# Kernel tuning notes

Hardware: AMD Instinct MI355X
Metric: run time of the kernel (lower is better)

Reference implementation:

```python
import jax, jax.numpy as jnp
import numpy as np

SIZES = [11793, 2948, 737, 184]   # vertices per mesh level, fine -> coarse
SPIRAL = [20, 14, 12, 9]          # spiral length per level
FILT = [128, 128, 64, 3]          # filters_dec[0]
LATENT = 128
BATCH = 16


def setup_inputs() -> dict:
    key = jax.random.key(0)
    ks = jax.random.split(key, 12)
    V = [s + 1 for s in SIZES]  # +1 dummy vertex per level
    inp = {}
    inp["z"] = jax.random.normal(ks[0], (BATCH, LATENT), jnp.float32)
    # dense upsampling matrices: level k+1 -> level k
    inp["U0"] = jax.random.normal(ks[1], (V[0], V[1]), jnp.float32) * 0.02
    inp["U1"] = jax.random.normal(ks[2], (V[1], V[2]), jnp.float32) * 0.02
    inp["U2"] = jax.random.normal(ks[3], (V[2], V[3]), jnp.float32) * 0.02
    # spiral index tables per level (shared across batch, values in [0, V))
    inp["S0"] = jax.random.randint(ks[4], (V[0], SPIRAL[0]), 0, V[0], dtype=jnp.int32)
    inp["S1"] = jax.random.randint(ks[5], (V[1], SPIRAL[1]), 0, V[1], dtype=jnp.int32)
    inp["S2"] = jax.random.randint(ks[6], (V[2], SPIRAL[2]), 0, V[2], dtype=jnp.int32)
    # fc_latent_dec: latent -> (sizes[-1]+1)*filters_dec[0][0]
    inp["Wfc"] = jax.random.normal(ks[7], (LATENT, V[3] * FILT[0]), jnp.float32) * 0.02
    inp["bfc"] = jnp.zeros((V[3] * FILT[0],), jnp.float32)
    # SpiralConv linear weights, stored (K*F_in, F_out), K-major flatten as in torch
    inp["W0"] = jax.random.normal(ks[8], (SPIRAL[2] * FILT[0], FILT[1]), jnp.float32) * 0.02
    inp["b0"] = jnp.zeros((FILT[1],), jnp.float32)
    inp["W1"] = jax.random.normal(ks[9], (SPIRAL[1] * FILT[1], FILT[2]), jnp.float32) * 0.02
    inp["b1"] = jnp.zeros((FILT[2],), jnp.float32)
    inp["W2"] = jax.random.normal(ks[10], (SPIRAL[0] * FILT[2], FILT[3]), jnp.float32) * 0.02
    inp["b2"] = jnp.zeros((FILT[3],), jnp.float32)
    return inp


def spiral_conv(x, S, W, b, elu):
    # x: (B, V, F); S: (V, K) vertex indices into the same level
    B, V, F = x.shape
    K = S.shape[1]
    g = jnp.take(x, S.reshape(-1), axis=1).reshape(B, V, K * F)  # gather, K-major flatten
    out = g @ W + b  # (B, V, F_out)
    if elu:
        out = jax.nn.elu(out)
    # zero out the dummy (last) vertex, as in Neural3DMM's zero_padding mask
    return out.at[:, -1, :].set(0.0)


def reference(z, U0, U1, U2, S0, S1, S2, Wfc, bfc, W0, b0, W1, b1, W2, b2):
    B = z.shape[0]
    x = (z @ Wfc + bfc).reshape(B, SIZES[-1] + 1, FILT[0])  # (B, 185, 128)
    x = jnp.einsum('vw,bwf->bvf', U2, x)                    # upsample -> (B, 738, 128)
    x = spiral_conv(x, S2, W0, b0, True)                    # (B, 738, 128)
    x = jnp.einsum('vw,bwf->bvf', U1, x)                    # (B, 2949, 128)
    x = spiral_conv(x, S1, W1, b1, True)                    # (B, 2949, 64)
    x = jnp.einsum('vw,bwf->bvf', U0, x)                    # (B, 11794, 64)
    x = spiral_conv(x, S0, W2, b2, False)                   # identity act -> (B, 11794, 3)
    return x
```

## Files before the change

### kernel.cpp

```cpp
#include <hip/hip_runtime.h>
#include <cmath>


#define NB 16

typedef __attribute__((ext_vector_type(8))) short bf16x8;
typedef __attribute__((ext_vector_type(4))) float f32x4;

__device__ __forceinline__ unsigned short f2bf(float x) {
    union { float f; unsigned u; } v; v.f = x;
    unsigned r = v.u + 0x7FFFu + ((v.u >> 16) & 1u);
    return (unsigned short)(r >> 16);
}
__device__ __forceinline__ void gload16(const void* src, void* dst) {
    __builtin_amdgcn_global_load_lds(
        (const __attribute__((address_space(1))) unsigned int*)src,
        (__attribute__((address_space(3))) unsigned int*)dst, 16, 0, 0);
}

__global__ __launch_bounds__(256) void cvt_ub(const float* __restrict__ src,
                                              unsigned short* __restrict__ dst,
                                              int V, int W, int Wp) {
    int k = blockIdx.x * 256 + threadIdx.x;
    int row = blockIdx.y;
    if (k >= Wp) return;
    float v = (row < V && k < W) ? src[(size_t)row * W + k] : 0.f;
    dst[(size_t)row * Wp + k] = f2bf(v);
}
__global__ __launch_bounds__(256) void cvt_wT(const float* __restrict__ w,
                                              unsigned short* __restrict__ wT,
                                              int K, int N, int total) {
    int id = blockIdx.x * 256 + threadIdx.x;
    if (id >= total) return;
    int n = id / K, k = id - n * K;
    wT[id] = f2bf(w[(size_t)k * N + n]);
}
__global__ __launch_bounds__(256) void cvt_w2(const float* __restrict__ w,
                                              unsigned short* __restrict__ wt) {
    int id = blockIdx.x * 256 + threadIdx.x;
    if (id >= 16 * 1288) return;
    int n = id / 1288, k = id - n * 1288;
    float v = (n < 3 && k < 1280) ? w[(size_t)k * 3 + n] : 0.f;
    wt[id] = f2bf(v);
}
__global__ __launch_bounds__(256) void cvt_sT(const int* __restrict__ S,
                                              int* __restrict__ ST,
                                              int V, int K, int total) {
    int id = blockIdx.x * 256 + threadIdx.x;
    if (id >= total) return;
    int k = id / V, v = id - k * V;
    ST[id] = S[(size_t)v * K + k];
}
__global__ __launch_bounds__(256) void zero16(int4* __restrict__ p, int n16) {
    int id = blockIdx.x * 256 + threadIdx.x;
    if (id < n16) p[id] = make_int4(0, 0, 0, 0);
}

__global__ __launch_bounds__(256) void fc_kernel(const float* __restrict__ z,
                                                 const float* __restrict__ Wfc,
                                                 const float* __restrict__ bfc,
                                                 unsigned short* __restrict__ x3T) {
    const int N = 185 * 128;
    __shared__ float zs[NB * 128];
    int t = threadIdx.x;
    for (int i = t; i < NB * 128; i += 256) zs[i] = z[i];
    __syncthreads();
    int n = blockIdx.x * 256 + t;
    if (n >= N) return;
    float acc[NB];
#pragma unroll
    for (int b = 0; b < NB; ++b) acc[b] = 0.f;
    for (int k = 0; k < 128; ++k) {
        float w = Wfc[k * N + n];
#pragma unroll
        for (int b = 0; b < NB; ++b) acc[b] = fmaf(zs[b * 128 + k], w, acc[b]);
    }
    float bv = bfc[n];
    int f = n & 127, v = n >> 7;
#pragma unroll
    for (int b = 0; b < NB; ++b)
        x3T[(size_t)(b * 128 + f) * 192 + v] = f2bf(acc[b] + bv);
}

template<int FSH, int VP>
__global__ __launch_bounds__(256) void ups_mfma(
    const unsigned short* __restrict__ Ub, const unsigned short* __restrict__ xT,
    unsigned short* __restrict__ out,
    int WpA, int WpB, int nsteps, int gxsh, int q) {
    const int F = 1 << FSH;
    __shared__ __align__(16) unsigned short As[3][128 * 32];
    __shared__ __align__(16) unsigned short Bs[3][128 * 32];
    const int t = threadIdx.x;
    const int wv = t >> 6, lane = t & 63;
    const int lr = lane & 15;

    const int flat = blockIdx.x;
    const int wg = (flat & 7) * q + (flat >> 3);
    const int m0 = (wg >> gxsh) * 128;
    const int n0 = (wg & ((1 << gxsh) - 1)) * 128;

    const int srow = lane >> 2;
    const int schunk = (((lane & 3) - ((lane >> 3) & 3)) & 3) * 8;
    const int ii0 = wv * 2, ii1 = wv * 2 + 1;
    const unsigned short* asrc0 = Ub + (size_t)(m0 + ii0 * 16 + srow) * WpA + schunk;
    const unsigned short* asrc1 = Ub + (size_t)(m0 + ii1 * 16 + srow) * WpA + schunk;
    const unsigned short* bsrc0 = xT + (size_t)(n0 + ii0 * 16 + srow) * WpB + schunk;
    const unsigned short* bsrc1 = xT + (size_t)(n0 + ii1 * 16 + srow) * WpB + schunk;

    const int fslot = (((lane >> 4) + (lr >> 1)) & 3) * 8;
    const int wrow = (wv >> 1) * 64;
    const int wcol = (wv & 1) * 64;
    const int u0 = wv * 1024;

    f32x4 acc[4][4];
#pragma unroll
    for (int i = 0; i < 4; ++i)
#pragma unroll
        for (int j = 0; j < 4; ++j) acc[i][j] = {0.f, 0.f, 0.f, 0.f};

#define UPS_STAGE(off_, B_)                                             \
    {                                                                   \
        gload16(asrc0 + (off_), &As[B_][u0]);                           \
        gload16(bsrc0 + (off_), &Bs[B_][u0]);                           \
        gload16(asrc1 + (off_), &As[B_][u0 + 512]);                     \
        gload16(bsrc1 + (off_), &Bs[B_][u0 + 512]);                     \
    }
#define UPS_COMPUTE(B_)                                                 \
    {                                                                   \
        bf16x8 af[4], bg[4];                                            \
        _Pragma("unroll")                                               \
        for (int mt = 0; mt < 4; ++mt)                                  \
            af[mt] = *(const bf16x8*)&As[B_][(wrow + mt * 16 + lr) * 32 + fslot]; \
        _Pragma("unroll")                                               \
        for (int nt = 0; nt < 4; ++nt)                                  \
            bg[nt] = *(const bf16x8*)&Bs[B_][(wcol + nt * 16 + lr) * 32 + fslot]; \
        _Pragma("unroll")                                               \
        for (int mt = 0; mt < 4; ++mt)                                  \
            _Pragma("unroll")                                           \
            for (int nt = 0; nt < 4; ++nt)                              \
                acc[mt][nt] = __builtin_amdgcn_mfma_f32_16x16x32_bf16(  \
                    af[mt], bg[nt], acc[mt][nt], 0, 0, 0);              \
    }
#define UPS_WAIT4 asm volatile("s_waitcnt vmcnt(4)" ::: "memory"); __builtin_amdgcn_s_barrier();
#define UPS_WAIT0 asm volatile("s_waitcnt vmcnt(0)" ::: "memory"); __builtin_amdgcn_s_barrier();

    UPS_STAGE(0, 0);
    UPS_STAGE(32, 1);
    UPS_WAIT4;

    const int m = nsteps / 3;
    for (int it = 0; it < m - 1; ++it) {
        UPS_STAGE(64, 2);  UPS_COMPUTE(0); UPS_WAIT4;
        UPS_STAGE(96, 0);  UPS_COMPUTE(1); UPS_WAIT4;
        UPS_STAGE(128, 1); UPS_COMPUTE(2); UPS_WAIT4;
        asrc0 += 96; asrc1 += 96; bsrc0 += 96; bsrc1 += 96;
    }
    UPS_STAGE(64, 2);
    UPS_COMPUTE(0); UPS_WAIT4;
    UPS_COMPUTE(1); UPS_WAIT0;
    UPS_COMPUTE(2);
#undef UPS_STAGE
#undef UPS_COMPUTE
#undef UPS_WAIT4
#undef UPS_WAIT0

#pragma unroll
    for (int mt = 0; mt < 4; ++mt) {
        const int vb = m0 + wrow + mt * 16 + (lane >> 4) * 4;
#pragma unroll
        for (int nt = 0; nt < 4; ++nt) {
            const int col = n0 + wcol + nt * 16 + lr;
            const int b = col >> FSH, f = col & (F - 1);
            unsigned short* op = out + (size_t)b * VP * F + f;
#pragma unroll
            for (int j = 0; j < 4; ++j)
                op[(size_t)(vb + j) * F] = f2bf(acc[mt][nt][j]);
        }
    }
}

template<int VP>
__global__ __launch_bounds__(64) void conv_mfma(
    const unsigned short* __restrict__ xu, const int* __restrict__ ST,
    const unsigned short* __restrict__ WT, const float* __restrict__ bias,
    unsigned short* __restrict__ outT,
    int VT, int Ksp, int Kdim, int nsteps, int Fout) {
    __shared__ __align__(16) unsigned short As[2][32 * 32];
    __shared__ __align__(16) unsigned short Bs[2][64 * 32];
    const int lane = threadIdx.x;
    const int lr = lane & 15;
    const int m0 = blockIdx.x * 32;
    const int n0 = blockIdx.y * 64;
    const int b = m0 / VP;
    const int v0 = m0 - b * VP;
    const unsigned short* xb = xu + (((size_t)b * VP) << 7);

    const int arow = lane >> 1;
    const int h = lane & 1;
    const int vg = (v0 + arow < VT) ? (v0 + arow) : (VT - 1);
    const int schunk = (((lane & 3) - ((lane >> 3) & 3)) & 3) * 8;
    const int fslot = (((lane >> 4) + (lr >> 1)) & 3) * 8;
    int sw0 = arow * 32 + (((2 * h + 0 + ((lane >> 2) & 3)) & 3) * 8);
    int sw1 = arow * 32 + (((2 * h + 1 + ((lane >> 2) & 3)) & 3) * 8);

    int s_c = 0;
    int idx_c = ST[vg];
    int idx_n = ST[(size_t)VT + vg];

    f32x4 acc[2][4];
#pragma unroll
    for (int i = 0; i < 2; ++i)
#pragma unroll
        for (int j = 0; j < 4; ++j) acc[i][j] = {0.f, 0.f, 0.f, 0.f};

#define CONV_COMPUTE(B_)                                                \
    {                                                                   \
        bf16x8 af[2], bg[4];                                            \
        _Pragma("unroll")                                               \
        for (int mt = 0; mt < 2; ++mt)                                  \
            af[mt] = *(const bf16x8*)&As[B_][(mt * 16 + lr) * 32 + fslot]; \
        _Pragma("unroll")                                               \
        for (int nt = 0; nt < 4; ++nt)                                  \
            bg[nt] = *(const bf16x8*)&Bs[B_][(nt * 16 + lr) * 32 + fslot]; \
        _Pragma("unroll")                                               \
        for (int mt = 0; mt < 2; ++mt)                                  \
            _Pragma("unroll")                                           \
            for (int nt = 0; nt < 4; ++nt)                              \
                acc[mt][nt] = __builtin_amdgcn_mfma_f32_16x16x32_bf16(  \
                    af[mt], bg[nt], acc[mt][nt], 0, 0, 0);              \
    }
#define CONV_BODY(tn_, CUR_, NXT_)                                      \
    {                                                                   \
        const int k0 = (tn_) * 32;                                      \
        const int sn = k0 >> 7;                                         \
        const int idx = (sn != s_c) ? idx_n : idx_c;                    \
        const unsigned short* p = xb + (((size_t)idx) << 7) + (k0 & 127) + h * 16; \
        bf16x8 g0 = *(const bf16x8*)(p);                                \
        bf16x8 g1 = *(const bf16x8*)(p + 8);                            \
        _Pragma("unroll")                                               \
        for (int i = 0; i < 4; ++i) {                                   \
            const int n = n0 + i * 16 + (lane >> 2);                    \
            gload16(WT + (size_t)n * Kdim + k0 + schunk, &Bs[NXT_][i * 512]); \
        }                                                               \
        if (sn != s_c) {                                                \
            idx_c = idx_n; s_c = sn;                                    \
            if (s_c + 1 < Ksp) idx_n = ST[(size_t)(s_c + 1) * VT + vg]; \
        }                                                               \
        CONV_COMPUTE(CUR_);                                             \
        *(bf16x8*)&As[NXT_][sw0] = g0;                                  \
        *(bf16x8*)&As[NXT_][sw1] = g1;                                  \
        __syncthreads();                                                \
    }

    {
        const unsigned short* p = xb + (((size_t)idx_c) << 7) + h * 16;
        bf16x8 g0 = *(const bf16x8*)(p);
        bf16x8 g1 = *(const bf16x8*)(p + 8);
#pragma unroll
        for (int i = 0; i < 4; ++i) {
            const int n = n0 + i * 16 + (lane >> 2);
            gload16(WT + (size_t)n * Kdim + schunk, &Bs[0][i * 512]);
        }
        *(bf16x8*)&As[0][sw0] = g0;
        *(bf16x8*)&As[0][sw1] = g1;
    }
    __syncthreads();

    for (int ts = 0; ts + 2 < nsteps; ts += 2) {
        CONV_BODY(ts + 1, 0, 1);
        CONV_BODY(ts + 2, 1, 0);
    }
    CONV_BODY(nsteps - 1, 0, 1);
    CONV_COMPUTE(1);
#undef CONV_BODY
#undef CONV_COMPUTE

#pragma unroll
    for (int nt = 0; nt < 4; ++nt) {
        const int n = n0 + nt * 16 + lr;
        const float bv = bias[n];
        unsigned short* op = outT + (size_t)(b * Fout + n) * VP;
#pragma unroll
        for (int mt = 0; mt < 2; ++mt) {
            const int v = v0 + mt * 16 + (lane >> 4) * 4;
            ushort4 stv;
#pragma unroll
            for (int j = 0; j < 4; ++j) {
                float val = acc[mt][nt][j] + bv;
                val = val > 0.f ? val : expm1f(val);
                if (v + j == VT - 1) val = 0.f;
                ((unsigned short*)&stv)[j] = f2bf(val);
            }
            *(ushort4*)(op + v) = stv;
        }
    }
}

__global__ __launch_bounds__(64) void out_mfma(
    const unsigned short* __restrict__ xu, const int* __restrict__ ST,
    const unsigned short* __restrict__ W2T, const float* __restrict__ b2,
    float* __restrict__ out) {
    const int VT = 11794, VP = 11904, TPB = 372;
    __shared__ __align__(16) unsigned short As[2][32 * 32];
    const int lane = threadIdx.x;
    const int lr = lane & 15;
    const int lko = (lane >> 4) * 8;
    const int bm = blockIdx.x;
    const int b = bm / TPB;
    const int v0 = (bm - b * TPB) * 32;
    const unsigned short* xb = xu + ((size_t)b * VP << 6);

    const int arow = lane >> 1;
    const int h = lane & 1;
    const int v = v0 + arow;
    const int vg = v < VT ? v : VT - 1;
    int sw0 = arow * 32 + (((2 * h + 0 + ((lane >> 2) & 3)) & 3) * 8);
    int sw1 = arow * 32 + (((2 * h + 1 + ((lane >> 2) & 3)) & 3) * 8);
    const int fslot = (((lane >> 4) + (lr >> 1)) & 3) * 8;

    int s_c = 0;
    int idx_c = ST[vg];
    int idx_n = ST[VT + vg];

    f32x4 acc[2];
    acc[0] = {0.f, 0.f, 0.f, 0.f};
    acc[1] = {0.f, 0.f, 0.f, 0.f};

    const unsigned short* wrow = W2T + (size_t)lr * 1288 + lko;
    bf16x8 bg_c = *(const bf16x8*)(wrow);

#define OUT_COMPUTE(B_)                                                 \
    {                                                                   \
        bf16x8 af[2];                                                   \
        _Pragma("unroll")                                               \
        for (int mt = 0; mt < 2; ++mt)                                  \
            af[mt] = *(const bf16x8*)&As[B_][(mt * 16 + lr) * 32 + fslot]; \
        _Pragma("unroll")                                               \
        for (int mt = 0; mt < 2; ++mt)                                  \
            acc[mt] = __builtin_amdgcn_mfma_f32_16x16x32_bf16(af[mt], bg_c, acc[mt], 0, 0, 0); \
    }
#define OUT_BODY(tn_, CUR_, NXT_)                                       \
    {                                                                   \
        const int k0 = (tn_) * 32;                                      \
        const int sn = k0 >> 6;                                         \
        const int idx = (sn != s_c) ? idx_n : idx_c;                    \
        const unsigned short* p = xb + (((size_t)idx) << 6) + (k0 & 63) + h * 16; \
        bf16x8 g0 = *(const bf16x8*)(p);                                \
        bf16x8 g1 = *(const bf16x8*)(p + 8);                            \
        bf16x8 bg_n = *(const bf16x8*)(wrow + k0);                      \
        if (sn != s_c) {                                                \
            idx_c = idx_n; s_c = sn;                                    \
            if (s_c + 1 < 20) idx_n = ST[(size_t)(s_c + 1) * VT + vg];  \
        }                                                               \
        OUT_COMPUTE(CUR_);                                              \
        bg_c = bg_n;                                                    \
        *(bf16x8*)&As[NXT_][sw0] = g0;                                  \
        *(bf16x8*)&As[NXT_][sw1] = g1;                                  \
        __syncthreads();                                                \
    }

    {
        const unsigned short* p = xb + ((size_t)idx_c << 6) + h * 16;
        bf16x8 g0 = *(const bf16x8*)(p);
        bf16x8 g1 = *(const bf16x8*)(p + 8);
        *(bf16x8*)&As[0][sw0] = g0;
        *(bf16x8*)&As[0][sw1] = g1;
    }
    __syncthreads();

    const int nsteps = 40;
    for (int ts = 0; ts + 2 < nsteps; ts += 2) {
        OUT_BODY(ts + 1, 0, 1);
        OUT_BODY(ts + 2, 1, 0);
    }
    OUT_BODY(nsteps - 1, 0, 1);
    OUT_COMPUTE(1);
#undef OUT_BODY
#undef OUT_COMPUTE

    if (lr < 3) {
        const float bv = b2[lr];
#pragma unroll
        for (int mt = 0; mt < 2; ++mt) {
#pragma unroll
            for (int j = 0; j < 4; ++j) {
                const int vv = v0 + mt * 16 + (lane >> 4) * 4 + j;
                if (vv < VT) {
                    float val = acc[mt][j] + bv;
                    if (vv == VT - 1) val = 0.f;
                    out[((size_t)b * VT + vv) * 3 + lr] = val;
                }
            }
        }
    }
}

extern "C" void kernel_launch(void* const* d_in, const int* in_sizes, int n_in,
                              void* d_out, int out_size, void* d_ws, size_t ws_size,
                              hipStream_t stream) {
    const float* z   = (const float*)d_in[0];
    const float* U0  = (const float*)d_in[1];
    const float* U1  = (const float*)d_in[2];
    const float* U2  = (const float*)d_in[3];
    const int*   S0  = (const int*)d_in[4];
    const int*   S1  = (const int*)d_in[5];
    const int*   S2  = (const int*)d_in[6];
    const float* Wfc = (const float*)d_in[7];
    const float* bfc = (const float*)d_in[8];
    const float* W0  = (const float*)d_in[9];
    const float* b0  = (const float*)d_in[10];
    const float* W1  = (const float*)d_in[11];
    const float* b1  = (const float*)d_in[12];
    const float* W2  = (const float*)d_in[13];
    const float* b2  = (const float*)d_in[14];
    float* out = (float*)d_out;

    char* ws = (char*)d_ws;
    unsigned short* Ub0 = (unsigned short*)(ws + 0);
    unsigned short* Ub1 = (unsigned short*)(ws + 70852608);
    unsigned short* Ub2 = (unsigned short*)(ws + 75571200);
    unsigned short* x3T = (unsigned short*)(ws + 75866112);
    unsigned short* x2u = (unsigned short*)(ws + 76652544);
    unsigned short* x2T = (unsigned short*)(ws + 79798272);
    unsigned short* x1u = (unsigned short*)(ws + 82944000);
    unsigned short* x1T = (unsigned short*)(ws + 95526912);
    unsigned short* x0u = (unsigned short*)(ws + 101818368);
    unsigned short* W0T = (unsigned short*)(ws + 126197760);
    unsigned short* W1T = (unsigned short*)(ws + 126590976);
    int* S1T = (int*)(ws + 126820352);
    int* S2T = (int*)(ws + 126985504);
    int* S0T = (int*)(ws + 127020928);
    unsigned short* W2T = (unsigned short*)(ws + 127964448);

    cvt_ub<<<dim3(12, 11904), 256, 0, stream>>>(U0, Ub0, 11794, 2949, 2976);
    cvt_ub<<<dim3(3, 3072), 256, 0, stream>>>(U1, Ub1, 2949, 738, 768);
    cvt_ub<<<dim3(1, 768), 256, 0, stream>>>(U2, Ub2, 738, 185, 192);
    cvt_wT<<<dim3((128 * 1536 + 255) / 256), 256, 0, stream>>>(W0, W0T, 1536, 128, 128 * 1536);
    cvt_wT<<<dim3((64 * 1792 + 255) / 256), 256, 0, stream>>>(W1, W1T, 1792, 64, 64 * 1792);
    cvt_w2<<<dim3((16 * 1288 + 255) / 256), 256, 0, stream>>>(W2, W2T);
    cvt_sT<<<dim3((14 * 2949 + 255) / 256), 256, 0, stream>>>(S1, S1T, 2949, 14, 14 * 2949);
    cvt_sT<<<dim3((12 * 738 + 255) / 256), 256, 0, stream>>>(S2, S2T, 738, 12, 12 * 738);
    cvt_sT<<<dim3((20 * 11794 + 255) / 256), 256, 0, stream>>>(S0, S0T, 11794, 20, 20 * 11794);
    zero16<<<dim3(192), 256, 0, stream>>>((int4*)x3T, 2048 * 192 * 2 / 16);

    fc_kernel<<<dim3((185 * 128 + 255) / 256), 256, 0, stream>>>(z, Wfc, bfc, x3T);
    ups_mfma<7, 768><<<dim3(96), 256, 0, stream>>>(Ub2, x3T, x2u, 192, 192, 6, 4, 12);
    conv_mfma<768><<<dim3(384, 2), 64, 0, stream>>>(x2u, S2T, W0T, b0, x2T, 738, 12, 1536, 48, 128);
    ups_mfma<7, 3072><<<dim3(384), 256, 0, stream>>>(Ub1, x2T, x1u, 768, 768, 24, 4, 48);
    conv_mfma<3072><<<dim3(1536, 1), 64, 0, stream>>>(x1u, S1T, W1T, b1, x1T, 2949, 14, 1792, 56, 64);
    ups_mfma<6, 11904><<<dim3(744), 256, 0, stream>>>(Ub0, x1T, x0u, 2976, 3072, 93, 3, 93);
    out_mfma<<<dim3(16 * 372), 64, 0, stream>>>(x0u, S0T, W2T, b2, out);
}
```

Before: 375.4 us.

## Replace LDS-staged spiral conv kernels with direct-register gather MFMA kernels

After: 420.2 us. 11.9% more time.

```diff
diff --git a/kernel.cpp b/kernel.cpp
--- a/kernel.cpp
+++ b/kernel.cpp
@@ -179,33 +179,25 @@
     }
 }
 
-template<int VP>
-__global__ __launch_bounds__(64) void conv_mfma(
+__global__ __launch_bounds__(256) void conv_nolds(
     const unsigned short* __restrict__ xu, const int* __restrict__ ST,
     const unsigned short* __restrict__ WT, const float* __restrict__ bias,
     unsigned short* __restrict__ outT,
-    int VT, int Ksp, int Kdim, int nsteps, int Fout) {
-    __shared__ __align__(16) unsigned short As[2][32 * 32];
-    __shared__ __align__(16) unsigned short Bs[2][64 * 32];
-    const int lane = threadIdx.x;
-    const int lr = lane & 15;
-    const int m0 = blockIdx.x * 32;
+    int VT, int VP, int Ksp, int Kdim, int Fout) {
+    const int t = threadIdx.x, wv = t >> 6, lane = t & 63;
+    const int lr = lane & 15, lko = (lane >> 4) * 8;
+    const int m0 = blockIdx.x * 128 + wv * 32;
     const int n0 = blockIdx.y * 64;
     const int b = m0 / VP;
     const int v0 = m0 - b * VP;
-    const unsigned short* xb = xu + (((size_t)b * VP) << 7);
-
-    const int arow = lane >> 1;
-    const int h = lane & 1;
-    const int vg = (v0 + arow < VT) ? (v0 + arow) : (VT - 1);
-    const int schunk = (((lane & 3) - ((lane >> 3) & 3)) & 3) * 8;
-    const int fslot = (((lane >> 4) + (lr >> 1)) & 3) * 8;
-    int sw0 = arow * 32 + (((2 * h + 0 + ((lane >> 2) & 3)) & 3) * 8);
-    int sw1 = arow * 32 + (((2 * h + 1 + ((lane >> 2) & 3)) & 3) * 8);
-
-    int s_c = 0;
-    int idx_c = ST[vg];
-    int idx_n = ST[(size_t)VT + vg];
+    const unsigned short* xb = xu + ((size_t)b * VP << 7);
+    const int r0 = v0 + lr, r1 = v0 + 16 + lr;
+    const int vg0 = r0 < VT ? r0 : VT - 1;
+    const int vg1 = r1 < VT ? r1 : VT - 1;
+    const unsigned short* wb0 = WT + (size_t)(n0 + lr) * Kdim + lko;
+    const unsigned short* wb1 = wb0 + (size_t)16 * Kdim;
+    const unsigned short* wb2 = wb0 + (size_t)32 * Kdim;
+    const unsigned short* wb3 = wb0 + (size_t)48 * Kdim;
 
     f32x4 acc[2][4];
 #pragma unroll
@@ -213,67 +205,36 @@
 #pragma unroll
         for (int j = 0; j < 4; ++j) acc[i][j] = {0.f, 0.f, 0.f, 0.f};
 
-#define CONV_COMPUTE(B_)                                                \
-    {                                                                   \
-        bf16x8 af[2], bg[4];                                            \
-        _Pragma("unroll")                                               \
-        for (int mt = 0; mt < 2; ++mt)                                  \
-            af[mt] = *(const bf16x8*)&As[B_][(mt * 16 + lr) * 32 + fslot]; \
-        _Pragma("unroll")                                               \
-        for (int nt = 0; nt < 4; ++nt)                                  \
-            bg[nt] = *(const bf16x8*)&Bs[B_][(nt * 16 + lr) * 32 + fslot]; \
-        _Pragma("unroll")                                               \
-        for (int mt = 0; mt < 2; ++mt)                                  \
-            _Pragma("unroll")                                           \
-            for (int nt = 0; nt < 4; ++nt)                              \
-                acc[mt][nt] = __builtin_amdgcn_mfma_f32_16x16x32_bf16(  \
-                    af[mt], bg[nt], acc[mt][nt], 0, 0, 0);              \
-    }
-#define CONV_BODY(tn_, CUR_, NXT_)                                      \
-    {                                                                   \
-        const int k0 = (tn_) * 32;                                      \
-        const int sn = k0 >> 7;                                         \
-        const int idx = (sn != s_c) ? idx_n : idx_c;                    \
-        const unsigned short* p = xb + (((size_t)idx) << 7) + (k0 & 127) + h * 16; \
-        bf16x8 g0 = *(const bf16x8*)(p);                                \
-        bf16x8 g1 = *(const bf16x8*)(p + 8);                            \
-        _Pragma("unroll")                                               \
-        for (int i = 0; i < 4; ++i) {                                   \
-            const int n = n0 + i * 16 + (lane >> 2);                    \
-            gload16(WT + (size_t)n * Kdim + k0 + schunk, &Bs[NXT_][i * 512]); \
-        }                                                               \
-        if (sn != s_c) {                                                \
-            idx_c = idx_n; s_c = sn;                                    \
-            if (s_c + 1 < Ksp) idx_n = ST[(size_t)(s_c + 1) * VT + vg]; \
-        }                                                               \
-        CONV_COMPUTE(CUR_);                                             \
-        *(bf16x8*)&As[NXT_][sw0] = g0;                                  \
-        *(bf16x8*)&As[NXT_][sw1] = g1;                                  \
-        __syncthreads();                                                \
-    }
-
-    {
-        const unsigned short* p = xb + (((size_t)idx_c) << 7) + h * 16;
-        bf16x8 g0 = *(const bf16x8*)(p);
-        bf16x8 g1 = *(const bf16x8*)(p + 8);
-#pragma unroll
-        for (int i = 0; i < 4; ++i) {
-            const int n = n0 + i * 16 + (lane >> 2);
-            gload16(WT + (size_t)n * Kdim + schunk, &Bs[0][i * 512]);
-        }
-        *(bf16x8*)&As[0][sw0] = g0;
-        *(bf16x8*)&As[0][sw1] = g1;
-    }
-    __syncthreads();
-
-    for (int ts = 0; ts + 2 < nsteps; ts += 2) {
-        CONV_BODY(ts + 1, 0, 1);
-        CONV_BODY(ts + 2, 1, 0);
-    }
-    CONV_BODY(nsteps - 1, 0, 1);
-    CONV_COMPUTE(1);
-#undef CONV_BODY
-#undef CONV_COMPUTE
+    int idx0 = ST[vg0];
+    int idx1 = ST[vg1];
+    for (int ks = 0; ks < Ksp; ++ks) {
+        int ni0 = idx0, ni1 = idx1;
+        if (ks + 1 < Ksp) {
+            ni0 = ST[(size_t)(ks + 1) * VT + vg0];
+            ni1 = ST[(size_t)(ks + 1) * VT + vg1];
+        }
+        const unsigned short* pa0 = xb + ((size_t)idx0 << 7) + lko;
+        const unsigned short* pa1 = xb + ((size_t)idx1 << 7) + lko;
+        const int kb = ks << 7;
+#pragma unroll
+        for (int sub = 0; sub < 4; ++sub) {
+            bf16x8 a0 = *(const bf16x8*)(pa0 + sub * 32);
+            bf16x8 a1 = *(const bf16x8*)(pa1 + sub * 32);
+            bf16x8 g0 = *(const bf16x8*)(wb0 + kb + sub * 32);
+            bf16x8 g1 = *(const bf16x8*)(wb1 + kb + sub * 32);
+            bf16x8 g2 = *(const bf16x8*)(wb2 + kb + sub * 32);
+            bf16x8 g3 = *(const bf16x8*)(wb3 + kb + sub * 32);
+            acc[0][0] = __builtin_amdgcn_mfma_f32_16x16x32_bf16(a0, g0, acc[0][0], 0, 0, 0);
+            acc[1][0] = __builtin_amdgcn_mfma_f32_16x16x32_bf16(a1, g0, acc[1][0], 0, 0, 0);
+            acc[0][1] = __builtin_amdgcn_mfma_f32_16x16x32_bf16(a0, g1, acc[0][1], 0, 0, 0);
+            acc[1][1] = __builtin_amdgcn_mfma_f32_16x16x32_bf16(a1, g1, acc[1][1], 0, 0, 0);
+            acc[0][2] = __builtin_amdgcn_mfma_f32_16x16x32_bf16(a0, g2, acc[0][2], 0, 0, 0);
+            acc[1][2] = __builtin_amdgcn_mfma_f32_16x16x32_bf16(a1, g2, acc[1][2], 0, 0, 0);
+            acc[0][3] = __builtin_amdgcn_mfma_f32_16x16x32_bf16(a0, g3, acc[0][3], 0, 0, 0);
+            acc[1][3] = __builtin_amdgcn_mfma_f32_16x16x32_bf16(a1, g3, acc[1][3], 0, 0, 0);
+        }
+        idx0 = ni0; idx1 = ni1;
+    }
 
 #pragma unroll
     for (int nt = 0; nt < 4; ++nt) {
@@ -296,92 +257,57 @@
     }
 }
 
-__global__ __launch_bounds__(64) void out_mfma(
+__global__ __launch_bounds__(256) void out_nolds(
     const unsigned short* __restrict__ xu, const int* __restrict__ ST,
     const unsigned short* __restrict__ W2T, const float* __restrict__ b2,
     float* __restrict__ out) {
-    const int VT = 11794, VP = 11904, TPB = 372;
-    __shared__ __align__(16) unsigned short As[2][32 * 32];
-    const int lane = threadIdx.x;
-    const int lr = lane & 15;
-    const int lko = (lane >> 4) * 8;
-    const int bm = blockIdx.x;
-    const int b = bm / TPB;
-    const int v0 = (bm - b * TPB) * 32;
+    const int VT = 11794, VP = 11904;
+    const int t = threadIdx.x, wv = t >> 6, lane = t & 63;
+    const int lr = lane & 15, lko = (lane >> 4) * 8;
+    const int m0 = blockIdx.x * 256 + wv * 64;
+    const int b = m0 / VP;
+    const int v0 = m0 - b * VP;
     const unsigned short* xb = xu + ((size_t)b * VP << 6);
-
-    const int arow = lane >> 1;
-    const int h = lane & 1;
-    const int v = v0 + arow;
-    const int vg = v < VT ? v : VT - 1;
-    int sw0 = arow * 32 + (((2 * h + 0 + ((lane >> 2) & 3)) & 3) * 8);
-    int sw1 = arow * 32 + (((2 * h + 1 + ((lane >> 2) & 3)) & 3) * 8);
-    const int fslot = (((lane >> 4) + (lr >> 1)) & 3) * 8;
-
-    int s_c = 0;
-    int idx_c = ST[vg];
-    int idx_n = ST[VT + vg];
-
-    f32x4 acc[2];
-    acc[0] = {0.f, 0.f, 0.f, 0.f};
-    acc[1] = {0.f, 0.f, 0.f, 0.f};
-
+    int vg[4];
+#pragma unroll
+    for (int mt = 0; mt < 4; ++mt) {
+        int r = v0 + mt * 16 + lr;
+        vg[mt] = r < VT ? r : VT - 1;
+    }
     const unsigned short* wrow = W2T + (size_t)lr * 1288 + lko;
-    bf16x8 bg_c = *(const bf16x8*)(wrow);
-
-#define OUT_COMPUTE(B_)                                                 \
-    {                                                                   \
-        bf16x8 af[2];                                                   \
-        _Pragma("unroll")                                               \
-        for (int mt = 0; mt < 2; ++mt)                                  \
-            af[mt] = *(const bf16x8*)&As[B_][(mt * 16 + lr) * 32 + fslot]; \
-        _Pragma("unroll")                                               \
-        for (int mt = 0; mt < 2; ++mt)                                  \
-            acc[mt] = __builtin_amdgcn_mfma_f32_16x16x32_bf16(af[mt], bg_c, acc[mt], 0, 0, 0); \
-    }
-#define OUT_BODY(tn_, CUR_, NXT_)                                       \
-    {                                                                   \
-        const int k0 = (tn_) * 32;                                      \
-        const int sn = k0 >> 6;                                         \
-        const int idx = (sn != s_c) ? idx_n : idx_c;                    \
-        const unsigned short* p = xb + (((size_t)idx) << 6) + (k0 & 63) + h * 16; \
-        bf16x8 g0 = *(const bf16x8*)(p);                                \
-        bf16x8 g1 = *(const bf16x8*)(p + 8);                            \
-        bf16x8 bg_n = *(const bf16x8*)(wrow + k0);                      \
-        if (sn != s_c) {                                                \
-            idx_c = idx_n; s_c = sn;                                    \
-            if (s_c + 1 < 20) idx_n = ST[(size_t)(s_c + 1) * VT + vg];  \
-        }                                                               \
-        OUT_COMPUTE(CUR_);                                              \
-        bg_c = bg_n;                                                    \
-        *(bf16x8*)&As[NXT_][sw0] = g0;                                  \
-        *(bf16x8*)&As[NXT_][sw1] = g1;                                  \
-        __syncthreads();                                                \
-    }
-
-    {
-        const unsigned short* p = xb + ((size_t)idx_c << 6) + h * 16;
-        bf16x8 g0 = *(const bf16x8*)(p);
-        bf16x8 g1 = *(const bf16x8*)(p + 8);
-        *(bf16x8*)&As[0][sw0] = g0;
-        *(bf16x8*)&As[0][sw1] = g1;
-    }
-    __syncthreads();
-
-    const int nsteps = 40;
-    for (int ts = 0; ts + 2 < nsteps; ts += 2) {
-        OUT_BODY(ts + 1, 0, 1);
-        OUT_BODY(ts + 2, 1, 0);
-    }
-    OUT_BODY(nsteps - 1, 0, 1);
-    OUT_COMPUTE(1);
-#undef OUT_BODY
-#undef OUT_COMPUTE
+
+    f32x4 acc[4];
+#pragma unroll
+    for (int i = 0; i < 4; ++i) acc[i] = {0.f, 0.f, 0.f, 0.f};
+
+    int i0 = ST[vg[0]], i1 = ST[vg[1]], i2 = ST[vg[2]], i3 = ST[vg[3]];
+    for (int ks = 0; ks < 20; ++ks) {
+        int n0i = i0, n1i = i1, n2i = i2, n3i = i3;
+        if (ks + 1 < 20) {
+            const int* srow = ST + (size_t)(ks + 1) * VT;
+            n0i = srow[vg[0]]; n1i = srow[vg[1]];
+            n2i = srow[vg[2]]; n3i = srow[vg[3]];
+        }
+        const int kb = ks << 6;
+#pragma unroll
+        for (int sub = 0; sub < 2; ++sub) {
+            bf16x8 bgv = *(const bf16x8*)(wrow + kb + sub * 32);
+            bf16x8 a0 = *(const bf16x8*)(xb + ((size_t)i0 << 6) + sub * 32 + lko);
+            bf16x8 a1 = *(const bf16x8*)(xb + ((size_t)i1 << 6) + sub * 32 + lko);
+            bf16x8 a2 = *(const bf16x8*)(xb + ((size_t)i2 << 6) + sub * 32 + lko);
+            bf16x8 a3 = *(const bf16x8*)(xb + ((size_t)i3 << 6) + sub * 32 + lko);
+            acc[0] = __builtin_amdgcn_mfma_f32_16x16x32_bf16(a0, bgv, acc[0], 0, 0, 0);
+            acc[1] = __builtin_amdgcn_mfma_f32_16x16x32_bf16(a1, bgv, acc[1], 0, 0, 0);
+            acc[2] = __builtin_amdgcn_mfma_f32_16x16x32_bf16(a2, bgv, acc[2], 0, 0, 0);
+            acc[3] = __builtin_amdgcn_mfma_f32_16x16x32_bf16(a3, bgv, acc[3], 0, 0, 0);
+        }
+        i0 = n0i; i1 = n1i; i2 = n2i; i3 = n3i;
+    }
 
     if (lr < 3) {
         const float bv = b2[lr];
 #pragma unroll
-        for (int mt = 0; mt < 2; ++mt) {
+        for (int mt = 0; mt < 4; ++mt) {
 #pragma unroll
             for (int j = 0; j < 4; ++j) {
                 const int vv = v0 + mt * 16 + (lane >> 4) * 4 + j;
@@ -445,9 +371,9 @@
 
     fc_kernel<<<dim3((185 * 128 + 255) / 256), 256, 0, stream>>>(z, Wfc, bfc, x3T);
     ups_mfma<7, 768><<<dim3(96), 256, 0, stream>>>(Ub2, x3T, x2u, 192, 192, 6, 4, 12);
-    conv_mfma<768><<<dim3(384, 2), 64, 0, stream>>>(x2u, S2T, W0T, b0, x2T, 738, 12, 1536, 48, 128);
+    conv_nolds<<<dim3(96, 2), 256, 0, stream>>>(x2u, S2T, W0T, b0, x2T, 738, 768, 12, 1536, 128);
     ups_mfma<7, 3072><<<dim3(384), 256, 0, stream>>>(Ub1, x2T, x1u, 768, 768, 24, 4, 48);
-    conv_mfma<3072><<<dim3(1536, 1), 64, 0, stream>>>(x1u, S1T, W1T, b1, x1T, 2949, 14, 1792, 56, 64);
+    conv_nolds<<<dim3(384, 1), 256, 0, stream>>>(x1u, S1T, W1T, b1, x1T, 2949, 3072, 14, 1792, 64);
     ups_mfma<6, 11904><<<dim3(744), 256, 0, stream>>>(Ub0, x1T, x0u, 2976, 3072, 93, 3, 93);
-    out_mfma<<<dim3(16 * 372), 64, 0, stream>>>(x0u, S0T, W2T, b2, out);
-}
+    out_nolds<<<dim3(744), 256, 0, stream>>>(x0u, S0T, W2T, b2, out);
+}
```
